# Kernel tuning notes

Measured on AMD Instinct MI355X. Metric: run time of the kernel, lower is better.

The kernel has to match this reference:

```python
import jax, jax.numpy as jnp
import numpy as np

EPS = 1e-5
NEG = -1e9  # stands in for -inf in the additive/boolean mask


def _layernorm(x, w, b):
    m = x.mean(-1, keepdims=True)
    v = ((x - m) ** 2).mean(-1, keepdims=True)
    return (x - m) / jnp.sqrt(v + EPS) * w + b


def _blocked_mask(n_vars, P, G):
    # True = attention blocked. Faithful vectorization of build_attention_mask
    # for a uniform num_patches_list ([P]*n_vars).
    T = P + G
    L = n_vars * T
    idx = jnp.arange(L)
    var = idx // T          # which variable each token belongs to
    pos = idx % T           # position within the variable's block
    is_patch = pos < P      # first P tokens are patch tokens, last G are global
    same_var = var[:, None] == var[None, :]
    # k == q branch: every query in the block attends the block's patch keys
    local = same_var & is_patch[None, :]
    # k != q branch: global token i attends global token i of other variables
    glob = (~same_var) & (~is_patch[:, None]) & (~is_patch[None, :]) & (pos[:, None] == pos[None, :])
    return ~(local | glob)


def setup_inputs() -> dict:
    key = jax.random.key(0)
    ks = jax.random.split(key, 12)
    B, D, Dff, H = 16, 512, 2048, 8
    n_vars, G, P = 7, 1, 128
    L = n_vars * (P + G)  # 903

    def init(k, shape, fan):
        return jax.random.normal(k, shape, jnp.float32) * (1.0 / np.sqrt(fan))

    x = jax.random.normal(ks[0], (B, L, D), jnp.float32)
    return {
        "x": x,
        "Wq": init(ks[1], (D, D), D), "bq": jnp.zeros((D,), jnp.float32),
        "Wk": init(ks[2], (D, D), D), "bk": jnp.zeros((D,), jnp.float32),
        "Wv": init(ks[3], (D, D), D), "bv": jnp.zeros((D,), jnp.float32),
        "Wo": init(ks[4], (D, D), D), "bo": jnp.zeros((D,), jnp.float32),
        "W1": init(ks[5], (D, Dff), D), "b1": jnp.zeros((Dff,), jnp.float32),
        "W2": init(ks[6], (Dff, D), Dff), "b2": jnp.zeros((D,), jnp.float32),
        "ln1_w": jnp.ones((D,), jnp.float32), "ln1_b": jnp.zeros((D,), jnp.float32),
        "ln2_w": jnp.ones((D,), jnp.float32), "ln2_b": jnp.zeros((D,), jnp.float32),
        "num_patches": P, "n_vars": n_vars, "num_global_tokens": G, "n_heads": H,
    }


def reference(x, Wq, bq, Wk, bk, Wv, bv, Wo, bo, W1, b1, W2, b2,
              ln1_w, ln1_b, ln2_w, ln2_b,
              num_patches, n_vars, num_global_tokens, n_heads):
    B, L, D = x.shape
    H = n_heads
    dh = D // H
    blocked = _blocked_mask(n_vars, num_patches, num_global_tokens)  # [L, L]

    # multi-head self-attention with block-sparse boolean mask
    q = (x @ Wq + bq).reshape(B, L, H, dh)
    k = (x @ Wk + bk).reshape(B, L, H, dh)
    v = (x @ Wv + bv).reshape(B, L, H, dh)
    scores = jnp.einsum('blhd,bshd->bhls', q, k) / np.sqrt(dh)
    scores = jnp.where(blocked[None, None], NEG, scores)
    A = jax.nn.softmax(scores, axis=-1)
    o = jnp.einsum('bhls,bshd->blhd', A, v).reshape(B, L, D)
    attn_out = o @ Wo + bo

    # residual + norm1, then 1x1-conv FFN (== per-token linear), residual + norm2
    x1 = _layernorm(x + attn_out, ln1_w, ln1_b)
    y = jax.nn.relu(x1 @ W1 + b1)
    y = y @ W2 + b2
    out = _layernorm(x1 + y, ln2_w, ln2_b)
    return out
```

## Files before the change

kernel.cpp:

```cpp
#include <hip/hip_runtime.h>

typedef __bf16 BF;
typedef __bf16 bf16x8 __attribute__((ext_vector_type(8)));
typedef float  f32x4  __attribute__((ext_vector_type(4)));

constexpr int B_   = 16;
constexpr int NV_  = 7;
constexpr int P_   = 128;
constexpr int G_   = 1;
constexpr int T_   = P_ + G_;
constexpr int L_   = NV_ * T_;
constexpr int D_   = 512;
constexpr int DFF_ = 2048;
constexpr int H_   = 8;
constexpr int DH_  = 64;
constexpr int M_   = B_ * L_;
constexpr int DQKV = 1536;

constexpr int TB_BQ = 0, TB_BK = 512, TB_BV = 1024, TB_BO = 1536;
constexpr int TB_B1 = 2048, TB_B2 = 4096;
constexpr int TB_LN1W = 4608, TB_LN1B = 5120, TB_LN2W = 5632, TB_LN2B = 6144;
constexpr int TB_TOTAL = 6656;

__device__ __forceinline__ bool probe_is_f32(const void* p) {
    return ((const unsigned short*)p)[0] == 0;
}
__device__ __forceinline__ float load_any(const void* p, size_t i, bool f32) {
    return f32 ? ((const float*)p)[i] : (float)((const BF*)p)[i];
}

__device__ __forceinline__ void gload_lds16(const BF* g, BF* l) {
    __builtin_amdgcn_global_load_lds(
        (const __attribute__((address_space(1))) void*)g,
        (__attribute__((address_space(3))) void*)l, 16, 0, 0);
}

__global__ __launch_bounds__(256)
void cvt2bf(const void* __restrict__ in, BF* __restrict__ out, int n,
            const void* __restrict__ probe) {
    const bool f32 = probe_is_f32(probe);
    for (size_t i = (size_t)blockIdx.x * 256 + threadIdx.x; i < (size_t)n;
         i += (size_t)gridDim.x * 256)
        out[i] = (BF)load_any(in, i, f32);
}

__global__ __launch_bounds__(256)
void cvt_small(const void* p0, const void* p1, const void* p2, const void* p3,
               const void* p4, const void* p5, const void* p6, const void* p7,
               const void* p8, const void* p9,
               BF* __restrict__ out, const void* __restrict__ probe) {
    const void* ptr[10] = {p0,p1,p2,p3,p4,p5,p6,p7,p8,p9};
    const int   off[10] = {TB_BQ,TB_BK,TB_BV,TB_BO,TB_B1,TB_B2,
                           TB_LN1W,TB_LN1B,TB_LN2W,TB_LN2B};
    const int   len[10] = {512,512,512,512,2048,512,512,512,512,512};
    const bool f32 = probe_is_f32(probe);
    const int i = blockIdx.x * 256 + threadIdx.x;
    if (i >= TB_TOTAL) return;
    #pragma unroll
    for (int s = 0; s < 10; ++s) {
        if (i < off[s] + len[s]) {
            out[i] = (BF)load_any(ptr[s], i - off[s], f32);
            return;
        }
    }
}

__global__ __launch_bounds__(256)
void transpose_cvt(const void* __restrict__ in, BF* __restrict__ out,
                   int R, int C, const void* __restrict__ probe) {
    __shared__ BF t[32][33];
    const bool f32 = probe_is_f32(probe);
    const int c0 = blockIdx.x * 32, r0 = blockIdx.y * 32;
    const int tx = threadIdx.x & 31, ty = threadIdx.x >> 5;
    #pragma unroll
    for (int i = ty; i < 32; i += 8)
        t[i][tx] = (BF)load_any(in, (size_t)(r0 + i) * C + c0 + tx, f32);
    __syncthreads();
    #pragma unroll
    for (int i = ty; i < 32; i += 8)
        out[(size_t)(c0 + i) * R + r0 + tx] = t[tx][i];
}

__global__ __launch_bounds__(256)
void transpose_cvt4(const void* __restrict__ w0, const void* __restrict__ w1,
                    const void* __restrict__ w2, const void* __restrict__ w3,
                    BF* __restrict__ out, const void* __restrict__ probe) {
    __shared__ BF t[32][33];
    const bool f32 = probe_is_f32(probe);
    const int z = blockIdx.z;
    const void* in = (z == 0) ? w0 : (z == 1) ? w1 : (z == 2) ? w2 : w3;
    BF* o = out + (size_t)z * D_ * D_;
    const int c0 = blockIdx.x * 32, r0 = blockIdx.y * 32;
    const int tx = threadIdx.x & 31, ty = threadIdx.x >> 5;
    #pragma unroll
    for (int i = ty; i < 32; i += 8)
        t[i][tx] = (BF)load_any(in, (size_t)(r0 + i) * D_ + c0 + tx, f32);
    __syncthreads();
    #pragma unroll
    for (int i = ty; i < 32; i += 8)
        o[(size_t)(c0 + i) * D_ + r0 + tx] = t[tx][i];
}

template<int RELU, int RES>
__global__ __launch_bounds__(256, 4)
void gemm_bt(const BF* __restrict__ A, const BF* __restrict__ Bt,
             const BF* __restrict__ bias, const BF* __restrict__ Res,
             BF* __restrict__ C, int M, int N, int K)
{
    __shared__ __align__(16) BF S[2 * 128 * 64];
    BF* As = S;
    BF* Bs = S + 128 * 64;

    const int tid  = threadIdx.x;
    const int lane = tid & 63;
    const int wave = tid >> 6;
    const int wm   = (wave >> 1) * 64;
    const int wn   = (wave & 1) * 64;

    const int nbx = gridDim.x;
    const int nb  = nbx * gridDim.y;
    const int lin = blockIdx.y * nbx + blockIdx.x;
    const int qq  = nb >> 3, rr = nb & 7;
    const int xcd = lin & 7, slot = lin >> 3;
    const int nl  = (xcd < rr) ? xcd * (qq + 1) + slot
                               : rr * (qq + 1) + (xcd - rr) * qq + slot;
    const long tileM = (long)(nl / nbx) * 128;
    const long tileN = (long)(nl % nbx) * 128;

    f32x4 acc[4][4] = {};

    const int srow = lane >> 3;
    const int scol = ((lane & 7) ^ srow) * 8;
    const int fm   = lane & 15;
    const int fkc  = lane >> 4;
    const int sw   = fm & 7;

    for (int k0 = 0; k0 < K; k0 += 64) {
        __syncthreads();
        #pragma unroll
        for (int c = 0; c < 4; ++c) {
            const int chunk = wave * 4 + c;
            const int row = chunk * 8 + srow;
            long ar = tileM + row; if (ar > (long)M - 1) ar = (long)M - 1;
            gload_lds16(A  + ar * K + k0 + scol, As + chunk * 512);
            const long br = tileN + row;
            gload_lds16(Bt + br * K + k0 + scol, Bs + chunk * 512);
        }
        __syncthreads();

        #pragma unroll
        for (int h = 0; h < 2; ++h) {
            const int kcs = ((h * 4 + fkc) ^ sw) * 8;
            bf16x8 af[4], bfr[4];
            #pragma unroll
            for (int i = 0; i < 4; ++i)
                af[i] = *(const bf16x8*)(As + (wm + i * 16 + fm) * 64 + kcs);
            #pragma unroll
            for (int j = 0; j < 4; ++j)
                bfr[j] = *(const bf16x8*)(Bs + (wn + j * 16 + fm) * 64 + kcs);
            #pragma unroll
            for (int i = 0; i < 4; ++i)
                #pragma unroll
                for (int j = 0; j < 4; ++j)
                    acc[i][j] = __builtin_amdgcn_mfma_f32_16x16x32_bf16(af[i], bfr[j], acc[i][j], 0, 0, 0);
        }
    }

    __syncthreads();
    const int rowb = (lane >> 4) * 4;
    #pragma unroll
    for (int j = 0; j < 4; ++j) {
        const long gcol = tileN + wn + j * 16 + fm;
        const float bv = (float)bias[gcol];
        #pragma unroll
        for (int i = 0; i < 4; ++i) {
            #pragma unroll
            for (int r = 0; r < 4; ++r) {
                float v2 = acc[i][j][r] + bv;
                if (RELU) v2 = fmaxf(v2, 0.0f);
                S[(wm + i * 16 + rowb + r) * 128 + wn + j * 16 + fm] = (BF)v2;
            }
        }
    }
    __syncthreads();
    #pragma unroll
    for (int it = 0; it < 8; ++it) {
        const int u = it * 256 + tid;
        const int row = u >> 4;
        const int c8  = (u & 15) * 8;
        const long grow = tileM + row;
        if (grow < M) {
            bf16x8 s8 = *(const bf16x8*)(S + row * 128 + c8);
            if (RES) {
                const bf16x8 rv = *(const bf16x8*)(Res + grow * (long)N + tileN + c8);
                #pragma unroll
                for (int e = 0; e < 8; ++e)
                    s8[e] = (BF)((float)s8[e] + (float)rv[e]);
            }
            *(bf16x8*)(C + grow * (long)N + tileN + c8) = s8;
        }
    }
}

__global__ __launch_bounds__(256)
void attn_kernel(const BF* __restrict__ qkv, BF* __restrict__ o)
{
    constexpr int LDK = 72;
    constexpr int LDP = 160;
    __shared__ __align__(16) BF Ks[144 * LDK];
    __shared__ __align__(16) BF Vt[DH_ * LDP];
    __shared__ __align__(16) BF Ps[4][16 * LDP];

    const int w = blockIdx.x, h = blockIdx.y, b = blockIdx.z;
    const int tid = threadIdx.x, wv = tid >> 6, lane = tid & 63;
    const size_t bRow  = (size_t)b * L_;
    const size_t qrow0 = bRow + (size_t)w * T_;
    const int    qoff  = h * DH_;

    for (int cidx = tid; cidx < 134 * 8; cidx += 256) {
        const int r = cidx >> 3, c8 = (cidx & 7) * 8;
        const int u = r - P_;
        const int key = (r < P_) ? (w * T_ + r) : ((u + (u >= w)) * T_ + P_);
        *(uint4*)(Ks + r * LDK + c8) =
            *(const uint4*)(qkv + (bRow + key) * DQKV + 512 + qoff + c8);
    }
    for (int cidx = tid; cidx < 160 * 8; cidx += 256) {
        const int r = cidx >> 3, c8 = (cidx & 7) * 8;
        bf16x8 tmp = {};
        if (r < 134) {
            const int u = r - P_;
            const int key = (r < P_) ? (w * T_ + r) : ((u + (u >= w)) * T_ + P_);
            tmp = *(const bf16x8*)(qkv + (bRow + key) * DQKV + 1024 + qoff + c8);
        }
        #pragma unroll
        for (int e = 0; e < 8; ++e) Vt[(c8 + e) * LDP + r] = tmp[e];
    }
    BF* Pw = &Ps[wv][0];
    if (lane < 32) {
        const uint4 z = {0, 0, 0, 0};
        *(uint4*)(Pw + (lane >> 1) * LDP + 144 + (lane & 1) * 8) = z;
    }
    __syncthreads();

    const int fm = lane & 15;
    const int fk = (lane >> 4) * 8;
    const int rowb_loc = (lane >> 4) * 4;

    for (int qt = wv; qt < 9; qt += 4) {
        int qr = qt * 16 + fm; if (qr > 128) qr = 128;
        const BF* qp = qkv + (qrow0 + qr) * DQKV + qoff + fk;
        const bf16x8 qf0 = *(const bf16x8*)qp;
        const bf16x8 qf1 = *(const bf16x8*)(qp + 32);

        f32x4 acc[9] = {};
        #pragma unroll
        for (int kt = 0; kt < 9; ++kt) {
            const BF* kp = Ks + (kt * 16 + fm) * LDK + fk;
            const bf16x8 kf0 = *(const bf16x8*)kp;
            const bf16x8 kf1 = *(const bf16x8*)(kp + 32);
            acc[kt] = __builtin_amdgcn_mfma_f32_16x16x32_bf16(qf0, kf0, acc[kt], 0, 0, 0);
            acc[kt] = __builtin_amdgcn_mfma_f32_16x16x32_bf16(qf1, kf1, acc[kt], 0, 0, 0);
        }

        #pragma unroll
        for (int r = 0; r < 4; ++r) {
            const int l = qt * 16 + rowb_loc + r;
            float sv[9];
            float mx = -1e30f;
            #pragma unroll
            for (int kt = 0; kt < 9; ++kt) {
                const int c = kt * 16 + fm;
                float s = acc[kt][r] * 0.125f;
                const bool ok = (c < 128) || (l == 128 && c < 134);
                s = ok ? s : -1e30f;
                sv[kt] = s;
                mx = fmaxf(mx, s);
            }
            #pragma unroll
            for (int off2 = 1; off2 < 16; off2 <<= 1)
                mx = fmaxf(mx, __shfl_xor(mx, off2, 64));
            float sum = 0.f;
            float pv[9];
            #pragma unroll
            for (int kt = 0; kt < 9; ++kt) { pv[kt] = __expf(sv[kt] - mx); sum += pv[kt]; }
            #pragma unroll
            for (int off2 = 1; off2 < 16; off2 <<= 1)
                sum += __shfl_xor(sum, off2, 64);
            const float inv = 1.0f / sum;
            #pragma unroll
            for (int kt = 0; kt < 9; ++kt)
                Pw[(rowb_loc + r) * LDP + kt * 16 + fm] = (BF)(pv[kt] * inv);
        }

        f32x4 oacc[4] = {};
        #pragma unroll
        for (int k32 = 0; k32 < 5; ++k32) {
            const bf16x8 pf = *(const bf16x8*)(Pw + fm * LDP + k32 * 32 + fk);
            #pragma unroll
            for (int nt = 0; nt < 4; ++nt) {
                const bf16x8 vf = *(const bf16x8*)(Vt + (nt * 16 + fm) * LDP + k32 * 32 + fk);
                oacc[nt] = __builtin_amdgcn_mfma_f32_16x16x32_bf16(pf, vf, oacc[nt], 0, 0, 0);
            }
        }

        #pragma unroll
        for (int nt = 0; nt < 4; ++nt) {
            #pragma unroll
            for (int r = 0; r < 4; ++r) {
                const int row = qt * 16 + rowb_loc + r;
                if (row <= 128)
                    o[(qrow0 + row) * D_ + qoff + nt * 16 + fm] = (BF)oacc[nt][r];
            }
        }
    }
}

template<int FINAL>
__global__ __launch_bounds__(256)
void ln_kernel(const BF* __restrict__ in, const BF* __restrict__ w,
               const BF* __restrict__ bias, void* __restrict__ out,
               const void* __restrict__ probe)
{
    const size_t base = (size_t)blockIdx.x * D_;
    const int tid = threadIdx.x;
    const float v0 = (float)in[base + tid];
    const float v1 = (float)in[base + tid + 256];
    float s  = v0 + v1;
    float q2 = v0 * v0 + v1 * v1;
    #pragma unroll
    for (int off = 32; off; off >>= 1) {
        s  += __shfl_xor(s,  off, 64);
        q2 += __shfl_xor(q2, off, 64);
    }
    __shared__ float ss[4], sq[4];
    if ((tid & 63) == 0) { ss[tid >> 6] = s; sq[tid >> 6] = q2; }
    __syncthreads();
    s  = ss[0] + ss[1] + ss[2] + ss[3];
    q2 = sq[0] + sq[1] + sq[2] + sq[3];
    const float mean = s * (1.0f / D_);
    const float var  = q2 * (1.0f / D_) - mean * mean;
    const float inv  = 1.0f / sqrtf(var + 1e-5f);
    const float r0 = (v0 - mean) * inv * (float)w[tid]       + (float)bias[tid];
    const float r1 = (v1 - mean) * inv * (float)w[tid + 256] + (float)bias[tid + 256];
    if (FINAL && probe_is_f32(probe)) {
        ((float*)out)[base + tid]       = r0;
        ((float*)out)[base + tid + 256] = r1;
    } else {
        ((BF*)out)[base + tid]       = (BF)r0;
        ((BF*)out)[base + tid + 256] = (BF)r1;
    }
}

extern "C" void kernel_launch(void* const* d_in, const int* in_sizes, int n_in,
                              void* d_out, int out_size, void* d_ws, size_t ws_size,
                              hipStream_t stream)
{
    const void* x_r    = d_in[0];
    const void* Wq_r   = d_in[1];
    const void* bq_r   = d_in[2];
    const void* Wk_r   = d_in[3];
    const void* bk_r   = d_in[4];
    const void* Wv_r   = d_in[5];
    const void* bv_r   = d_in[6];
    const void* Wo_r   = d_in[7];
    const void* bo_r   = d_in[8];
    const void* W1_r   = d_in[9];
    const void* b1_r   = d_in[10];
    const void* W2_r   = d_in[11];
    const void* b2_r   = d_in[12];
    const void* ln1w_r = d_in[13];
    const void* ln1b_r = d_in[14];
    const void* ln2w_r = d_in[15];
    const void* ln2b_r = d_in[16];
    const void* probe  = ln1w_r;

    BF* ws = (BF*)d_ws;
    const size_t MD = (size_t)M_ * D_;
    BF* xc    = ws;
    BF* qkv   = ws + MD;
    BF* ob    = ws + 4 * MD;
    BF* zb    = ws + 5 * MD;
    BF* WqkvT = ws + 6 * MD;
    BF* WoT   = WqkvT + 3 * (size_t)D_ * D_;
    BF* W1T   = WqkvT + 4 * (size_t)D_ * D_;
    BF* W2T   = W1T   + (size_t)D_ * DFF_;
    BF* tail  = W2T   + (size_t)DFF_ * D_;

    BF* aob = qkv;
    BF* x1b = xc;
    BF* hid = qkv;

    const dim3 blk(256);

    cvt2bf<<<dim3(2048), blk, 0, stream>>>(x_r, xc, (int)MD, probe);
    cvt_small<<<dim3((TB_TOTAL + 255) / 256), blk, 0, stream>>>(
        bq_r, bk_r, bv_r, bo_r, b1_r, b2_r, ln1w_r, ln1b_r, ln2w_r, ln2b_r, tail, probe);
    transpose_cvt4<<<dim3(D_ / 32, D_ / 32, 4), blk, 0, stream>>>(
        Wq_r, Wk_r, Wv_r, Wo_r, WqkvT, probe);
    transpose_cvt<<<dim3(DFF_ / 32, D_ / 32), blk, 0, stream>>>(W1_r, W1T, D_, DFF_, probe);
    transpose_cvt<<<dim3(D_ / 32, DFF_ / 32), blk, 0, stream>>>(W2_r, W2T, DFF_, D_, probe);

    const int MT = (M_ + 127) / 128;

    gemm_bt<0,0><<<dim3(DQKV / 128, MT), blk, 0, stream>>>(
        xc, WqkvT, tail + TB_BQ, nullptr, qkv, M_, DQKV, D_);

    attn_kernel<<<dim3(NV_, H_, B_), blk, 0, stream>>>(qkv, ob);

    gemm_bt<0,1><<<dim3(D_ / 128, MT), blk, 0, stream>>>(
        ob, WoT, tail + TB_BO, xc, aob, M_, D_, D_);

    ln_kernel<0><<<dim3(M_), blk, 0, stream>>>(
        aob, tail + TB_LN1W, tail + TB_LN1B, x1b, probe);

    gemm_bt<1,0><<<dim3(DFF_ / 128, MT), blk, 0, stream>>>(
        x1b, W1T, tail + TB_B1, nullptr, hid, M_, DFF_, D_);
    gemm_bt<0,1><<<dim3(D_ / 128, MT), blk, 0, stream>>>(
        hid, W2T, tail + TB_B2, x1b, zb, M_, D_, DFF_);

    ln_kernel<1><<<dim3(M_), blk, 0, stream>>>(
        zb, tail + TB_LN2W, tail + TB_LN2B, d_out, probe);
}
```

Before: 326.5 us.

## Add double-buffered LDS GEMM with XCD-aware tile remap for N=512 GEMMs

Adds a GEMM variant that double-buffers the A/B LDS tiles so the global-to-LDS loads for the next K-slice overlap the MFMA compute on the current one. Block indices are also remapped so consecutive tiles land on the same XCD, which should improve L2 reuse. The Wo projection and W2 FFN GEMMs, which have narrow N=512 grids and few blocks, now use this kernel. The cost is twice the LDS per block, which can limit occupancy. The kernel also assumes K is a multiple of 128.

```diff
diff --git a/kernel.cpp b/kernel.cpp
--- a/kernel.cpp
+++ b/kernel.cpp
@@ -191,6 +191,125 @@
         const long grow = tileM + row;
         if (grow < M) {
             bf16x8 s8 = *(const bf16x8*)(S + row * 128 + c8);
+            if (RES) {
+                const bf16x8 rv = *(const bf16x8*)(Res + grow * (long)N + tileN + c8);
+                #pragma unroll
+                for (int e = 0; e < 8; ++e)
+                    s8[e] = (BF)((float)s8[e] + (float)rv[e]);
+            }
+            *(bf16x8*)(C + grow * (long)N + tileN + c8) = s8;
+        }
+    }
+}
+
+template<int RELU, int RES>
+__global__ __launch_bounds__(256, 2)
+void gemm_bt_db(const BF* __restrict__ A, const BF* __restrict__ Bt,
+                const BF* __restrict__ bias, const BF* __restrict__ Res,
+                BF* __restrict__ C, int M, int N, int K)
+{
+    __shared__ __align__(16) BF S[2][2 * 128 * 64];
+
+    const int tid  = threadIdx.x;
+    const int lane = tid & 63;
+    const int wave = tid >> 6;
+    const int wm   = (wave >> 1) * 64;
+    const int wn   = (wave & 1) * 64;
+
+    const int nbx = gridDim.x;
+    const int nb  = nbx * gridDim.y;
+    const int lin = blockIdx.y * nbx + blockIdx.x;
+    const int qq  = nb >> 3, rr = nb & 7;
+    const int xcd = lin & 7, slot = lin >> 3;
+    const int nl  = (xcd < rr) ? xcd * (qq + 1) + slot
+                               : rr * (qq + 1) + (xcd - rr) * qq + slot;
+    const long tileM = (long)(nl / nbx) * 128;
+    const long tileN = (long)(nl % nbx) * 128;
+
+    f32x4 acc[4][4] = {};
+
+    const int srow = lane >> 3;
+    const int scol = ((lane & 7) ^ srow) * 8;
+    const int fm   = lane & 15;
+    const int fkc  = lane >> 4;
+    const int sw   = fm & 7;
+
+    auto STAGE = [&](BF* buf, int k0) {
+        BF* As_ = buf;
+        BF* Bs_ = buf + 128 * 64;
+        #pragma unroll
+        for (int c = 0; c < 4; ++c) {
+            const int chunk = wave * 4 + c;
+            const int row = chunk * 8 + srow;
+            long ar = tileM + row; if (ar > (long)M - 1) ar = (long)M - 1;
+            gload_lds16(A  + ar * K + k0 + scol, As_ + chunk * 512);
+            const long br = tileN + row;
+            gload_lds16(Bt + br * K + k0 + scol, Bs_ + chunk * 512);
+        }
+        __builtin_amdgcn_sched_barrier(0);
+    };
+    auto COMPUTE = [&](const BF* buf) {
+        const BF* As_ = buf;
+        const BF* Bs_ = buf + 128 * 64;
+        #pragma unroll
+        for (int h = 0; h < 2; ++h) {
+            const int kcs = ((h * 4 + fkc) ^ sw) * 8;
+            bf16x8 af[4], bfr[4];
+            #pragma unroll
+            for (int i = 0; i < 4; ++i)
+                af[i] = *(const bf16x8*)(As_ + (wm + i * 16 + fm) * 64 + kcs);
+            #pragma unroll
+            for (int j = 0; j < 4; ++j)
+                bfr[j] = *(const bf16x8*)(Bs_ + (wn + j * 16 + fm) * 64 + kcs);
+            #pragma unroll
+            for (int i = 0; i < 4; ++i)
+                #pragma unroll
+                for (int j = 0; j < 4; ++j)
+                    acc[i][j] = __builtin_amdgcn_mfma_f32_16x16x32_bf16(af[i], bfr[j], acc[i][j], 0, 0, 0);
+        }
+    };
+
+    const int NT = K >> 6;
+    STAGE(S[0], 0);
+    __syncthreads();
+    for (int kp = 0; kp < NT - 2; kp += 2) {
+        STAGE(S[1], (kp + 1) << 6);
+        COMPUTE(S[0]);
+        __syncthreads();
+        STAGE(S[0], (kp + 2) << 6);
+        COMPUTE(S[1]);
+        __syncthreads();
+    }
+    STAGE(S[1], (NT - 1) << 6);
+    COMPUTE(S[0]);
+    __syncthreads();
+    COMPUTE(S[1]);
+
+    const int rowb = (lane >> 4) * 4;
+    BF* Ct = &S[0][0];
+    #pragma unroll
+    for (int j = 0; j < 4; ++j) {
+        const long gcol = tileN + wn + j * 16 + fm;
+        const float bv = (float)bias[gcol];
+        #pragma unroll
+        for (int i = 0; i < 4; ++i) {
+            #pragma unroll
+            for (int r = 0; r < 4; ++r) {
+                float v2 = acc[i][j][r] + bv;
+                if (RELU) v2 = fmaxf(v2, 0.0f);
+                Ct[(wm + i * 16 + rowb + r) * 128 + wn + j * 16 + fm] = (BF)v2;
+            }
+        }
+    }
+    __syncthreads();
+    #pragma unroll
+    for (int it = 0; it < 8; ++it) {
+        const int u = it * 256 + tid;
+        const int row = u >> 4;
+        const int c8  = (u & 15) * 8;
+        const long grow = tileM + row;
+        if (grow < M) {
+            bf16x8 s8 = *(const bf16x8*)(Ct + row * 128 + c8);
             if (RES) {
                 const bf16x8 rv = *(const bf16x8*)(Res + grow * (long)N + tileN + c8);
                 #pragma unroll
@@ -407,7 +526,7 @@
 
     attn_kernel<<<dim3(NV_, H_, B_), blk, 0, stream>>>(qkv, ob);
 
-    gemm_bt<0,1><<<dim3(D_ / 128, MT), blk, 0, stream>>>(
+    gemm_bt_db<0,1><<<dim3(D_ / 128, MT), blk, 0, stream>>>(
         ob, WoT, tail + TB_BO, xc, aob, M_, D_, D_);
 
     ln_kernel<0><<<dim3(M_), blk, 0, stream>>>(
@@ -415,7 +534,7 @@
 
     gemm_bt<1,0><<<dim3(DFF_ / 128, MT), blk, 0, stream>>>(
         x1b, W1T, tail + TB_B1, nullptr, hid, M_, DFF_, D_);
-    gemm_bt<0,1><<<dim3(D_ / 128, MT), blk, 0, stream>>>(
+    gemm_bt_db<0,1><<<dim3(D_ / 128, MT), blk, 0, stream>>>(
         hid, W2T, tail + TB_B2, x1b, zb, M_, D_, DFF_);
 
     ln_kernel<1><<<dim3(M_), blk, 0, stream>>>(
```

After: 307.6 us. 5.8% less time.

## Double-buffer LDS tiles in GEMM to overlap global loads with MFMA

Applied to the files above, without the earlier changes.

Replaces the single-buffered GEMM main loop with a two-stage ping-pong LDS pipeline. The next K-tile is issued into the alternate buffer while MFMAs consume the current one, and one of the two barriers per iteration is dropped. This is meant to hide global-to-LDS load latency. LDS use doubles to 64KB per block and launch bounds drop from 4 to 2 blocks per CU, so there is less occupancy to hide latency the other way.

```diff
diff --git a/kernel.cpp b/kernel.cpp
--- a/kernel.cpp
+++ b/kernel.cpp
@@ -102,14 +102,12 @@
 }
 
 template<int RELU, int RES>
-__global__ __launch_bounds__(256, 4)
-void gemm_bt(const BF* __restrict__ A, const BF* __restrict__ Bt,
-             const BF* __restrict__ bias, const BF* __restrict__ Res,
-             BF* __restrict__ C, int M, int N, int K)
+__global__ __launch_bounds__(256, 2)
+void gemm_bt_db(const BF* __restrict__ A, const BF* __restrict__ Bt,
+                const BF* __restrict__ bias, const BF* __restrict__ Res,
+                BF* __restrict__ C, int M, int N, int K)
 {
-    __shared__ __align__(16) BF S[2 * 128 * 64];
-    BF* As = S;
-    BF* Bs = S + 128 * 64;
+    __shared__ __align__(16) BF S[2][2 * 128 * 64];
 
     const int tid  = threadIdx.x;
     const int lane = tid & 63;
@@ -135,39 +133,59 @@
     const int fkc  = lane >> 4;
     const int sw   = fm & 7;
 
-    for (int k0 = 0; k0 < K; k0 += 64) {
-        __syncthreads();
+    auto STAGE = [&](BF* buf, int k0) {
+        BF* As_ = buf;
+        BF* Bs_ = buf + 128 * 64;
         #pragma unroll
         for (int c = 0; c < 4; ++c) {
             const int chunk = wave * 4 + c;
             const int row = chunk * 8 + srow;
             long ar = tileM + row; if (ar > (long)M - 1) ar = (long)M - 1;
-            gload_lds16(A  + ar * K + k0 + scol, As + chunk * 512);
+            gload_lds16(A  + ar * K + k0 + scol, As_ + chunk * 512);
             const long br = tileN + row;
-            gload_lds16(Bt + br * K + k0 + scol, Bs + chunk * 512);
-        }
-        __syncthreads();
-
+            gload_lds16(Bt + br * K + k0 + scol, Bs_ + chunk * 512);
+        }
+        __builtin_amdgcn_sched_barrier(0);
+    };
+    auto COMPUTE = [&](const BF* buf) {
+        const BF* As_ = buf;
+        const BF* Bs_ = buf + 128 * 64;
         #pragma unroll
         for (int h = 0; h < 2; ++h) {
             const int kcs = ((h * 4 + fkc) ^ sw) * 8;
             bf16x8 af[4], bfr[4];
             #pragma unroll
             for (int i = 0; i < 4; ++i)
-                af[i] = *(const bf16x8*)(As + (wm + i * 16 + fm) * 64 + kcs);
+                af[i] = *(const bf16x8*)(As_ + (wm + i * 16 + fm) * 64 + kcs);
             #pragma unroll
             for (int j = 0; j < 4; ++j)
-                bfr[j] = *(const bf16x8*)(Bs + (wn + j * 16 + fm) * 64 + kcs);
+                bfr[j] = *(const bf16x8*)(Bs_ + (wn + j * 16 + fm) * 64 + kcs);
             #pragma unroll
             for (int i = 0; i < 4; ++i)
                 #pragma unroll
                 for (int j = 0; j < 4; ++j)
                     acc[i][j] = __builtin_amdgcn_mfma_f32_16x16x32_bf16(af[i], bfr[j], acc[i][j], 0, 0, 0);
         }
-    }
-
-    __syncthreads();
+    };
+
+    const int NT = K >> 6;
+    STAGE(S[0], 0);
+    __syncthreads();
+    for (int kp = 0; kp < NT - 2; kp += 2) {
+        STAGE(S[1], (kp + 1) << 6);
+        COMPUTE(S[0]);
+        __syncthreads();
+        STAGE(S[0], (kp + 2) << 6);
+        COMPUTE(S[1]);
+        __syncthreads();
+    }
+    STAGE(S[1], (NT - 1) << 6);
+    COMPUTE(S[0]);
+    __syncthreads();
+    COMPUTE(S[1]);
+
     const int rowb = (lane >> 4) * 4;
+    BF* Ct = &S[0][0];
     #pragma unroll
     for (int j = 0; j < 4; ++j) {
         const long gcol = tileN + wn + j * 16 + fm;
@@ -178,7 +196,7 @@
             for (int r = 0; r < 4; ++r) {
                 float v2 = acc[i][j][r] + bv;
                 if (RELU) v2 = fmaxf(v2, 0.0f);
-                S[(wm + i * 16 + rowb + r) * 128 + wn + j * 16 + fm] = (BF)v2;
+                Ct[(wm + i * 16 + rowb + r) * 128 + wn + j * 16 + fm] = (BF)v2;
             }
         }
     }
@@ -190,7 +208,7 @@
         const int c8  = (u & 15) * 8;
         const long grow = tileM + row;
         if (grow < M) {
-            bf16x8 s8 = *(const bf16x8*)(S + row * 128 + c8);
+            bf16x8 s8 = *(const bf16x8*)(Ct + row * 128 + c8);
             if (RES) {
                 const bf16x8 rv = *(const bf16x8*)(Res + grow * (long)N + tileN + c8);
                 #pragma unroll
@@ -402,20 +420,20 @@
 
     const int MT = (M_ + 127) / 128;
 
-    gemm_bt<0,0><<<dim3(DQKV / 128, MT), blk, 0, stream>>>(
+    gemm_bt_db<0,0><<<dim3(DQKV / 128, MT), blk, 0, stream>>>(
         xc, WqkvT, tail + TB_BQ, nullptr, qkv, M_, DQKV, D_);
 
     attn_kernel<<<dim3(NV_, H_, B_), blk, 0, stream>>>(qkv, ob);
 
-    gemm_bt<0,1><<<dim3(D_ / 128, MT), blk, 0, stream>>>(
+    gemm_bt_db<0,1><<<dim3(D_ / 128, MT), blk, 0, stream>>>(
         ob, WoT, tail + TB_BO, xc, aob, M_, D_, D_);
 
     ln_kernel<0><<<dim3(M_), blk, 0, stream>>>(
         aob, tail + TB_LN1W, tail + TB_LN1B, x1b, probe);
 
-    gemm_bt<1,0><<<dim3(DFF_ / 128, MT), blk, 0, stream>>>(
+    gemm_bt_db<1,0><<<dim3(DFF_ / 128, MT), blk, 0, stream>>>(
         x1b, W1T, tail + TB_B1, nullptr, hid, M_, DFF_, D_);
-    gemm_bt<0,1><<<dim3(D_ / 128, MT), blk, 0, stream>>>(
+    gemm_bt_db<0,1><<<dim3(D_ / 128, MT), blk, 0, stream>>>(
         hid, W2T, tail + TB_B2, x1b, zb, M_, D_, DFF_);
 
     ln_kernel<1><<<dim3(M_), blk, 0, stream>>>(
```

Result: faster. 314.2 us (-3.8%).
